# Kernel optimization log

Hardware: AMD Instinct MI355X
Metric: run time of the kernel (lower is better)

The kernel has to match this reference:

```python
import jax, jax.numpy as jnp
import numpy as np

B, S, D, H = 4, 2048, 768, 12
HD = D // H  # head_dim = 64


def setup_inputs() -> dict:
    key = jax.random.key(0)
    k1, k2, k3, k4, k5 = jax.random.split(key, 5)
    scale = 0.02
    return {
        "x": jax.random.normal(k1, (B, S, D), dtype=jnp.float32),
        "w_qkv": jax.random.normal(k2, (D, 3 * D), dtype=jnp.float32) * scale,
        "b_qkv": jax.random.normal(k3, (3 * D,), dtype=jnp.float32) * scale,
        "w_proj": jax.random.normal(k4, (D, D), dtype=jnp.float32) * scale,
        "b_proj": jax.random.normal(k5, (D,), dtype=jnp.float32) * scale,
    }


def reference(x, w_qkv, b_qkv, w_proj, b_proj):
    b, s, d = x.shape
    # fused qkv projection: (b, s, 3d) -> (3, b, h, s, hd)
    qkv = x @ w_qkv + b_qkv
    qkv = qkv.reshape(b, s, 3, H, HD).transpose(2, 0, 3, 1, 4)
    q, k, v = qkv[0], qkv[1], qkv[2]
    # scaled dot-product attention with explicit (b, h, s, s) scores
    scores = jnp.einsum("bhqd,bhkd->bhqk", q, k) / jnp.sqrt(jnp.float32(HD))
    attn = jax.nn.softmax(scores, axis=-1)
    out = jnp.einsum("bhqk,bhkd->bhqd", attn, v)
    out = out.transpose(0, 2, 1, 3).reshape(b, s, d)  # concat heads
    return out @ w_proj + b_proj
```

## Files before the change

### kernel.cpp

```cpp
#include <hip/hip_runtime.h>
#include <hip/hip_bf16.h>
#include <stdint.h>


typedef __attribute__((ext_vector_type(8))) short bf16x8;
typedef __attribute__((ext_vector_type(4))) float f32x4;
typedef __attribute__((ext_vector_type(4))) unsigned short u16x4;

__device__ __forceinline__ unsigned short f2bf(float x) {
  union { float f; uint32_t u; } v; v.f = x;
  uint32_t r = v.u + 0x7FFF + ((v.u >> 16) & 1);
  return (unsigned short)(r >> 16);
}

__device__ __forceinline__ uint32_t cvtpk_bf16(float lo, float hi) {
  uint32_t r;
  asm("v_cvt_pk_bf16_f32 %0, %1, %2" : "=v"(r) : "v"(lo), "v"(hi));
  return r;
}

__device__ __forceinline__ void gload_lds16(const void* g, void* l) {
  __builtin_amdgcn_global_load_lds(
      (const __attribute__((address_space(1))) void*)g,
      (__attribute__((address_space(3))) void*)l, 16, 0, 0);
}

__global__ void cast_x_kernel(const float* __restrict__ x,
                              unsigned short* __restrict__ xb, int n) {
  int idx = (blockIdx.x * blockDim.x + threadIdx.x) * 4;
  if (idx < n) {
    f32x4 v = *(const f32x4*)(x + idx);
    u16x4 o;
    o[0] = f2bf(v[0]); o[1] = f2bf(v[1]); o[2] = f2bf(v[2]); o[3] = f2bf(v[3]);
    *(u16x4*)(xb + idx) = o;
  }
}

__global__ void transpose_cast_kernel(const float* __restrict__ W,
                                      unsigned short* __restrict__ Wt,
                                      int K, int N) {
  __shared__ float tile[64][65];
  int k0 = blockIdx.y * 64, n0 = blockIdx.x * 64;
  int t = threadIdx.x;
#pragma unroll
  for (int i = 0; i < 16; i++) {
    int idx = i * 256 + t; int r = idx >> 6, c = idx & 63;
    tile[r][c] = W[(size_t)(k0 + r) * N + n0 + c];
  }
  __syncthreads();
#pragma unroll
  for (int i = 0; i < 16; i++) {
    int idx = i * 256 + t; int r = idx >> 6, c = idx & 63;
    Wt[(size_t)(n0 + r) * K + k0 + c] = f2bf(tile[c][r]);
  }
}

template <int EPI>
__global__ __launch_bounds__(256, 2) void gemm_kernel(
    const unsigned short* __restrict__ A,
    const unsigned short* __restrict__ Bt,
    const float* __restrict__ bias,
    void* __restrict__ out0,
    unsigned short* __restrict__ Kb,
    unsigned short* __restrict__ Vt,
    int M, int N, int K) {
  __shared__ unsigned short As[128 * 64];
  __shared__ unsigned short Bs[128 * 64];
  const int tid = threadIdx.x;
  const int wave = tid >> 6, lane = tid & 63;
  const int wm = wave >> 1, wn = wave & 1;
  const int m0 = blockIdx.y * 128, n0 = blockIdx.x * 128;
  const int g = lane >> 4, c16 = lane & 15;
  f32x4 acc[4][4] = {};

  for (int k0 = 0; k0 < K; k0 += 64) {
    int rb = wave * 32;
#pragma unroll
    for (int j = 0; j < 4; j++) {
      int r = rb + j * 8 + (lane >> 3);
      int ca = (lane & 7) ^ (r & 7);
      gload_lds16(A + (size_t)(m0 + r) * K + k0 + ca * 8, As + (rb + j * 8) * 64);
      gload_lds16(Bt + (size_t)(n0 + r) * K + k0 + ca * 8, Bs + (rb + j * 8) * 64);
    }
    __syncthreads();
#pragma unroll
    for (int ks = 0; ks < 2; ks++) {
      bf16x8 af[4], bfr[4];
#pragma unroll
      for (int mi = 0; mi < 4; mi++) {
        int row = wm * 64 + mi * 16 + c16;
        int ch = (ks * 4 + g) ^ (row & 7);
        af[mi] = *(const bf16x8*)(As + row * 64 + ch * 8);
      }
#pragma unroll
      for (int nj = 0; nj < 4; nj++) {
        int row = wn * 64 + nj * 16 + c16;
        int ch = (ks * 4 + g) ^ (row & 7);
        bfr[nj] = *(const bf16x8*)(Bs + row * 64 + ch * 8);
      }
#pragma unroll
      for (int mi = 0; mi < 4; mi++)
#pragma unroll
        for (int nj = 0; nj < 4; nj++)
          acc[mi][nj] = __builtin_amdgcn_mfma_f32_16x16x32_bf16(
              af[mi], bfr[nj], acc[mi][nj], 0, 0, 0);
    }
    __syncthreads();
  }

  if (EPI == 0) {
    const float QSC = 0.125f * 1.44269504088896f;
    unsigned short* Qb = (unsigned short*)out0;
#pragma unroll
    for (int nj = 0; nj < 4; nj++) {
      int n = n0 + wn * 64 + nj * 16 + c16;
      int t = n / 768, rr = n % 768;
      int h = rr >> 6, d = rr & 63;
      float bv = bias[n];
#pragma unroll
      for (int mi = 0; mi < 4; mi++) {
        int mrow = m0 + wm * 64 + mi * 16 + g * 4;
        int b = mrow >> 11, s = mrow & 2047;
        if (t == 0) {
          size_t base = ((size_t)(b * 12 + h) * 2048 + s) * 64 + d;
#pragma unroll
          for (int rg = 0; rg < 4; rg++)
            Qb[base + (size_t)rg * 64] = f2bf((acc[mi][nj][rg] + bv) * QSC);
        } else if (t == 1) {
          size_t base = ((size_t)(b * 12 + h) * 2048 + s) * 64 + d;
#pragma unroll
          for (int rg = 0; rg < 4; rg++)
            Kb[base + (size_t)rg * 64] = f2bf(acc[mi][nj][rg] + bv);
        } else {
          u16x4 p;
          p[0] = f2bf(acc[mi][nj][0] + bv);
          p[1] = f2bf(acc[mi][nj][1] + bv);
          p[2] = f2bf(acc[mi][nj][2] + bv);
          p[3] = f2bf(acc[mi][nj][3] + bv);
          *(u16x4*)(Vt + ((size_t)(b * 12 + h) * 64 + d) * 2048 + s) = p;
        }
      }
    }
  } else {
    float* outp = (float*)out0;
#pragma unroll
    for (int nj = 0; nj < 4; nj++) {
      int n = n0 + wn * 64 + nj * 16 + c16;
      float bv = bias[n];
#pragma unroll
      for (int mi = 0; mi < 4; mi++) {
        int mrow = m0 + wm * 64 + mi * 16 + g * 4;
#pragma unroll
        for (int rg = 0; rg < 4; rg++)
          outp[(size_t)(mrow + rg) * N + n] = acc[mi][nj][rg] + bv;
      }
    }
  }
}

__global__ __launch_bounds__(256, 4) void attn_kernel(
    const unsigned short* __restrict__ Qb,
    const unsigned short* __restrict__ Kb,
    const unsigned short* __restrict__ Vt,
    unsigned short* __restrict__ Ao) {
  __shared__ unsigned short Ks[64 * 64];
  __shared__ unsigned short Vs[64 * 64];
  __shared__ unsigned short Ps[4][2][16 * 72];
  const int bh = blockIdx.y;
  const int q0 = blockIdx.x * 128;
  const int tid = threadIdx.x;
  const int wave = tid >> 6, lane = tid & 63;
  const int g = lane >> 4, c16 = lane & 15;

  bf16x8 qf[2][2];
  {
    const unsigned short* qp =
        Qb + ((size_t)bh * 2048 + q0 + wave * 32 + c16) * 64;
#pragma unroll
    for (int qa = 0; qa < 2; qa++) {
      qf[qa][0] = *(const bf16x8*)(qp + qa * 1024 + g * 8);
      qf[qa][1] = *(const bf16x8*)(qp + qa * 1024 + 32 + g * 8);
    }
  }
  f32x4 acc_o[2][4] = {};
  float l_run[2] = {0.f, 0.f};
  const int alane = (lane & 48) + g * 4;
  const int rb = wave * 16;

  for (int kt = 0; kt < 32; kt++) {
#pragma unroll
    for (int j = 0; j < 2; j++) {
      int r = rb + j * 8 + (lane >> 3);
      int ca = (lane & 7) ^ (r & 7);
      gload_lds16(Kb + ((size_t)bh * 2048 + kt * 64 + r) * 64 + ca * 8,
                  Ks + (rb + j * 8) * 64);
      gload_lds16(Vt + ((size_t)bh * 64 + r) * 2048 + kt * 64 + ca * 8,
                  Vs + (rb + j * 8) * 64);
    }
    __syncthreads();

    f32x4 sacc[2][4] = {};
#pragma unroll
    for (int ks = 0; ks < 2; ks++) {
#pragma unroll
      for (int nf = 0; nf < 4; nf++) {
        int row = nf * 16 + c16;
        int ch = (ks * 4 + g) ^ (row & 7);
        bf16x8 kf = *(const bf16x8*)(Ks + row * 64 + ch * 8);
        sacc[0][nf] =
            __builtin_amdgcn_mfma_f32_16x16x32_bf16(kf, qf[0][ks], sacc[0][nf], 0, 0, 0);
        sacc[1][nf] =
            __builtin_amdgcn_mfma_f32_16x16x32_bf16(kf, qf[1][ks], sacc[1][nf], 0, 0, 0);
      }
    }

#pragma unroll
    for (int qa = 0; qa < 2; qa++) {
      float rs = 0.f;
#pragma unroll
      for (int nf = 0; nf < 4; nf++) {
        float e0 = __builtin_amdgcn_exp2f(sacc[qa][nf][0]);
        float e1 = __builtin_amdgcn_exp2f(sacc[qa][nf][1]);
        float e2 = __builtin_amdgcn_exp2f(sacc[qa][nf][2]);
        float e3 = __builtin_amdgcn_exp2f(sacc[qa][nf][3]);
        rs += (e0 + e1) + (e2 + e3);
        uint32_t w0 = cvtpk_bf16(e0, e1);
        uint32_t w1 = cvtpk_bf16(e2, e3);
        *(uint64_t*)(&Ps[wave][qa][c16 * 72 + nf * 16 + g * 4]) =
            (uint64_t)w0 | ((uint64_t)w1 << 32);
      }
      rs += __shfl_xor(rs, 16);
      rs += __shfl_xor(rs, 32);
      l_run[qa] += rs;
    }

#pragma unroll
    for (int ks = 0; ks < 2; ks++) {
      bf16x8 paf0 = *(const bf16x8*)(&Ps[wave][0][c16 * 72 + ks * 32 + g * 8]);
      bf16x8 paf1 = *(const bf16x8*)(&Ps[wave][1][c16 * 72 + ks * 32 + g * 8]);
#pragma unroll
      for (int nf = 0; nf < 4; nf++) {
        int row = nf * 16 + c16;
        int ch = (ks * 4 + g) ^ (row & 7);
        bf16x8 vf = *(const bf16x8*)(Vs + row * 64 + ch * 8);
        acc_o[0][nf] =
            __builtin_amdgcn_mfma_f32_16x16x32_bf16(paf0, vf, acc_o[0][nf], 0, 0, 0);
        acc_o[1][nf] =
            __builtin_amdgcn_mfma_f32_16x16x32_bf16(paf1, vf, acc_o[1][nf], 0, 0, 0);
      }
    }
    __syncthreads();
  }

  const int b = bh / 12, h = bh % 12;
#pragma unroll
  for (int qa = 0; qa < 2; qa++) {
    float l_q[4];
#pragma unroll
    for (int rg = 0; rg < 4; rg++)
      l_q[rg] = __shfl(l_run[qa], alane + rg);
#pragma unroll
    for (int nf = 0; nf < 4; nf++) {
#pragma unroll
      for (int rg = 0; rg < 4; rg++) {
        float v = acc_o[qa][nf][rg] / l_q[rg];
        int srow = q0 + wave * 32 + qa * 16 + g * 4 + rg;
        Ao[((size_t)(b * 2048 + srow)) * 768 + h * 64 + nf * 16 + c16] = f2bf(v);
      }
    }
  }
}

extern "C" void kernel_launch(void* const* d_in, const int* in_sizes, int n_in,
                              void* d_out, int out_size, void* d_ws, size_t ws_size,
                              hipStream_t stream) {
  const float* x      = (const float*)d_in[0];
  const float* w_qkv  = (const float*)d_in[1];
  const float* b_qkv  = (const float*)d_in[2];
  const float* w_proj = (const float*)d_in[3];
  const float* b_proj = (const float*)d_in[4];

  unsigned short* xb  = (unsigned short*)d_ws;
  unsigned short* wqt = xb + 6291456;
  unsigned short* wpt = wqt + 1769472;
  unsigned short* Qb  = wpt + 589824;
  unsigned short* Kb  = Qb + 6291456;
  unsigned short* Vt  = Kb + 6291456;
  unsigned short* Ao  = Vt + 6291456;

  cast_x_kernel<<<6144, 256, 0, stream>>>(x, xb, 6291456);
  transpose_cast_kernel<<<dim3(36, 12), 256, 0, stream>>>(w_qkv, wqt, 768, 2304);
  transpose_cast_kernel<<<dim3(12, 12), 256, 0, stream>>>(w_proj, wpt, 768, 768);

  gemm_kernel<0><<<dim3(18, 64), 256, 0, stream>>>(
      xb, wqt, b_qkv, (void*)Qb, Kb, Vt, 8192, 2304, 768);

  attn_kernel<<<dim3(16, 48), 256, 0, stream>>>(Qb, Kb, Vt, Ao);

  gemm_kernel<1><<<dim3(6, 64), 256, 0, stream>>>(
      Ao, wpt, b_proj, d_out, nullptr, nullptr, 8192, 768, 768);
}
```

Baseline: 154.0 us.

## Double-buffer K/V tiles in attention kernel to overlap loads with compute

```diff
diff --git a/kernel.cpp b/kernel.cpp
--- a/kernel.cpp
+++ b/kernel.cpp
@@ -163,14 +163,19 @@
     const unsigned short* __restrict__ Kb,
     const unsigned short* __restrict__ Vt,
     unsigned short* __restrict__ Ao) {
-  __shared__ unsigned short Ks[64 * 64];
-  __shared__ unsigned short Vs[64 * 64];
+  __shared__ unsigned short Ks[2][64 * 64];
+  __shared__ unsigned short Vs[2][64 * 64];
   __shared__ unsigned short Ps[4][2][16 * 72];
   const int bh = blockIdx.y;
   const int q0 = blockIdx.x * 128;
   const int tid = threadIdx.x;
   const int wave = tid >> 6, lane = tid & 63;
   const int g = lane >> 4, c16 = lane & 15;
+  const int rb = wave * 16;
+
+  const int sr = rb + (lane >> 3);
+  const int sca = (lane & 7) ^ (sr & 7);
+  const int sca1 = (lane & 7) ^ ((sr + 8) & 7);
 
   bf16x8 qf[2][2];
   {
@@ -185,19 +190,29 @@
   f32x4 acc_o[2][4] = {};
   float l_run[2] = {0.f, 0.f};
   const int alane = (lane & 48) + g * 4;
-  const int rb = wave * 16;
+
+  {
+    const unsigned short* kp = Kb + ((size_t)bh * 2048 + sr) * 64;
+    const unsigned short* vp = Vt + ((size_t)bh * 64 + sr) * 2048;
+    gload_lds16(kp + sca * 8, &Ks[0][(rb)*64]);
+    gload_lds16(kp + 8 * 64 + sca1 * 8, &Ks[0][(rb + 8) * 64]);
+    gload_lds16(vp + sca * 8, &Vs[0][(rb)*64]);
+    gload_lds16(vp + 8 * 2048 + sca1 * 8, &Vs[0][(rb + 8) * 64]);
+  }
+  __syncthreads();
 
   for (int kt = 0; kt < 32; kt++) {
-#pragma unroll
-    for (int j = 0; j < 2; j++) {
-      int r = rb + j * 8 + (lane >> 3);
-      int ca = (lane & 7) ^ (r & 7);
-      gload_lds16(Kb + ((size_t)bh * 2048 + kt * 64 + r) * 64 + ca * 8,
-                  Ks + (rb + j * 8) * 64);
-      gload_lds16(Vt + ((size_t)bh * 64 + r) * 2048 + kt * 64 + ca * 8,
-                  Vs + (rb + j * 8) * 64);
-    }
-    __syncthreads();
+    const int cur = kt & 1;
+    if (kt < 31) {
+      const unsigned short* kp =
+          Kb + ((size_t)bh * 2048 + (kt + 1) * 64 + sr) * 64;
+      const unsigned short* vp =
+          Vt + ((size_t)bh * 64 + sr) * 2048 + (kt + 1) * 64;
+      gload_lds16(kp + sca * 8, &Ks[cur ^ 1][(rb)*64]);
+      gload_lds16(kp + 8 * 64 + sca1 * 8, &Ks[cur ^ 1][(rb + 8) * 64]);
+      gload_lds16(vp + sca * 8, &Vs[cur ^ 1][(rb)*64]);
+      gload_lds16(vp + 8 * 2048 + sca1 * 8, &Vs[cur ^ 1][(rb + 8) * 64]);
+    }
 
     f32x4 sacc[2][4] = {};
 #pragma unroll
@@ -206,7 +221,7 @@
       for (int nf = 0; nf < 4; nf++) {
         int row = nf * 16 + c16;
         int ch = (ks * 4 + g) ^ (row & 7);
-        bf16x8 kf = *(const bf16x8*)(Ks + row * 64 + ch * 8);
+        bf16x8 kf = *(const bf16x8*)(&Ks[cur][row * 64 + ch * 8]);
         sacc[0][nf] =
             __builtin_amdgcn_mfma_f32_16x16x32_bf16(kf, qf[0][ks], sacc[0][nf], 0, 0, 0);
         sacc[1][nf] =
@@ -242,7 +257,7 @@
       for (int nf = 0; nf < 4; nf++) {
         int row = nf * 16 + c16;
         int ch = (ks * 4 + g) ^ (row & 7);
-        bf16x8 vf = *(const bf16x8*)(Vs + row * 64 + ch * 8);
+        bf16x8 vf = *(const bf16x8*)(&Vs[cur][row * 64 + ch * 8]);
         acc_o[0][nf] =
             __builtin_amdgcn_mfma_f32_16x16x32_bf16(paf0, vf, acc_o[0][nf], 0, 0, 0);
         acc_o[1][nf] =
```

Result: slower. 165.7 us (+7.6%).

## Double-buffer K/V tiles in attention kernel to overlap loads with compute

Applied to the files above, without the earlier changes.

```diff
diff --git a/kernel.cpp b/kernel.cpp
--- a/kernel.cpp
+++ b/kernel.cpp
@@ -158,19 +158,31 @@
   }
 }
 
-__global__ __launch_bounds__(256, 4) void attn_kernel(
+struct AttnState {
+  f32x4 acc_o[2][4];
+  float l_run[2];
+};
+
+__global__ __launch_bounds__(256, 3) void attn_kernel(
     const unsigned short* __restrict__ Qb,
     const unsigned short* __restrict__ Kb,
     const unsigned short* __restrict__ Vt,
     unsigned short* __restrict__ Ao) {
-  __shared__ unsigned short Ks[64 * 64];
-  __shared__ unsigned short Vs[64 * 64];
+  __shared__ unsigned short Ks0[64 * 64];
+  __shared__ unsigned short Ks1[64 * 64];
+  __shared__ unsigned short Vs0[64 * 64];
+  __shared__ unsigned short Vs1[64 * 64];
   __shared__ unsigned short Ps[4][2][16 * 72];
   const int bh = blockIdx.y;
   const int q0 = blockIdx.x * 128;
   const int tid = threadIdx.x;
   const int wave = tid >> 6, lane = tid & 63;
   const int g = lane >> 4, c16 = lane & 15;
+  const int rb = wave * 16;
+
+  const int sr = rb + (lane >> 3);
+  const int sca = (lane & 7) ^ (sr & 7);
+  const int sca1 = (lane & 7) ^ ((sr + 8) & 7);
 
   bf16x8 qf[2][2];
   {
@@ -185,72 +197,80 @@
   f32x4 acc_o[2][4] = {};
   float l_run[2] = {0.f, 0.f};
   const int alane = (lane & 48) + g * 4;
-  const int rb = wave * 16;
-
-  for (int kt = 0; kt < 32; kt++) {
-#pragma unroll
-    for (int j = 0; j < 2; j++) {
-      int r = rb + j * 8 + (lane >> 3);
-      int ca = (lane & 7) ^ (r & 7);
-      gload_lds16(Kb + ((size_t)bh * 2048 + kt * 64 + r) * 64 + ca * 8,
-                  Ks + (rb + j * 8) * 64);
-      gload_lds16(Vt + ((size_t)bh * 64 + r) * 2048 + kt * 64 + ca * 8,
-                  Vs + (rb + j * 8) * 64);
-    }
+
+  const unsigned short* kp = Kb + ((size_t)bh * 2048 + sr) * 64;
+  const unsigned short* vp = Vt + ((size_t)bh * 64 + sr) * 2048;
+
+#define STAGE_KV(KS, VS)                                   \
+  do {                                                     \
+    gload_lds16(kp + sca * 8, &KS[rb * 64]);               \
+    gload_lds16(kp + 8 * 64 + sca1 * 8, &KS[(rb + 8) * 64]); \
+    gload_lds16(vp + sca * 8, &VS[rb * 64]);               \
+    gload_lds16(vp + 8 * 2048 + sca1 * 8, &VS[(rb + 8) * 64]); \
+    kp += 64 * 64;                                         \
+    vp += 64;                                              \
+  } while (0)
+
+#define ATTN_TILE(KS, VS)                                                     \
+  do {                                                                        \
+    f32x4 sacc[2][4] = {};                                                    \
+    _Pragma("unroll") for (int ks = 0; ks < 2; ks++) {                        \
+      _Pragma("unroll") for (int nf = 0; nf < 4; nf++) {                      \
+        int row = nf * 16 + c16;                                              \
+        int ch = (ks * 4 + g) ^ (row & 7);                                    \
+        bf16x8 kf = *(const bf16x8*)(&KS[row * 64 + ch * 8]);                 \
+        sacc[0][nf] = __builtin_amdgcn_mfma_f32_16x16x32_bf16(                \
+            kf, qf[0][ks], sacc[0][nf], 0, 0, 0);                             \
+        sacc[1][nf] = __builtin_amdgcn_mfma_f32_16x16x32_bf16(                \
+            kf, qf[1][ks], sacc[1][nf], 0, 0, 0);                             \
+      }                                                                       \
+    }                                                                         \
+    _Pragma("unroll") for (int qa = 0; qa < 2; qa++) {                        \
+      float rs = 0.f;                                                         \
+      _Pragma("unroll") for (int nf = 0; nf < 4; nf++) {                      \
+        float e0 = __builtin_amdgcn_exp2f(sacc[qa][nf][0]);                   \
+        float e1 = __builtin_amdgcn_exp2f(sacc[qa][nf][1]);                   \
+        float e2 = __builtin_amdgcn_exp2f(sacc[qa][nf][2]);                   \
+        float e3 = __builtin_amdgcn_exp2f(sacc[qa][nf][3]);                   \
+        rs += (e0 + e1) + (e2 + e3);                                          \
+        uint32_t w0 = cvtpk_bf16(e0, e1);                                     \
+        uint32_t w1 = cvtpk_bf16(e2, e3);                                     \
+        *(uint64_t*)(&Ps[wave][qa][c16 * 72 + nf * 16 + g * 4]) =             \
+            (uint64_t)w0 | ((uint64_t)w1 << 32);                              \
+      }                                                                       \
+      rs += __shfl_xor(rs, 16);                                               \
+      rs += __shfl_xor(rs, 32);                                               \
+      l_run[qa] += rs;                                                        \
+    }                                                                         \
+    _Pragma("unroll") for (int ks = 0; ks < 2; ks++) {                        \
+      bf16x8 paf0 = *(const bf16x8*)(&Ps[wave][0][c16 * 72 + ks * 32 + g * 8]); \
+      bf16x8 paf1 = *(const bf16x8*)(&Ps[wave][1][c16 * 72 + ks * 32 + g * 8]); \
+      _Pragma("unroll") for (int nf = 0; nf < 4; nf++) {                      \
+        int row = nf * 16 + c16;                                              \
+        int ch = (ks * 4 + g) ^ (row & 7);                                    \
+        bf16x8 vf = *(const bf16x8*)(&VS[row * 64 + ch * 8]);                 \
+        acc_o[0][nf] = __builtin_amdgcn_mfma_f32_16x16x32_bf16(               \
+            paf0, vf, acc_o[0][nf], 0, 0, 0);                                 \
+        acc_o[1][nf] = __builtin_amdgcn_mfma_f32_16x16x32_bf16(               \
+            paf1, vf, acc_o[1][nf], 0, 0, 0);                                 \
+      }                                                                       \
+    }                                                                         \
+  } while (0)
+
+  STAGE_KV(Ks0, Vs0);
+  __syncthreads();
+
+  for (int kt2 = 0; kt2 < 16; kt2++) {
+    STAGE_KV(Ks1, Vs1);
+    ATTN_TILE(Ks0, Vs0);
     __syncthreads();
 
-    f32x4 sacc[2][4] = {};
-#pragma unroll
-    for (int ks = 0; ks < 2; ks++) {
-#pragma unroll
-      for (int nf = 0; nf < 4; nf++) {
-        int row = nf * 16 + c16;
-        int ch = (ks * 4 + g) ^ (row & 7);
-        bf16x8 kf = *(const bf16x8*)(Ks + row * 64 + ch * 8);
-        sacc[0][nf] =
-            __builtin_amdgcn_mfma_f32_16x16x32_bf16(kf, qf[0][ks], sacc[0][nf], 0, 0, 0);
-        sacc[1][nf] =
-            __builtin_amdgcn_mfma_f32_16x16x32_bf16(kf, qf[1][ks], sacc[1][nf], 0, 0, 0);
-      }
-    }
-
-#pragma unroll
-    for (int qa = 0; qa < 2; qa++) {
-      float rs = 0.f;
-#pragma unroll
-      for (int nf = 0; nf < 4; nf++) {
-        float e0 = __builtin_amdgcn_exp2f(sacc[qa][nf][0]);
-        float e1 = __builtin_amdgcn_exp2f(sacc[qa][nf][1]);
-        float e2 = __builtin_amdgcn_exp2f(sacc[qa][nf][2]);
-        float e3 = __builtin_amdgcn_exp2f(sacc[qa][nf][3]);
-        rs += (e0 + e1) + (e2 + e3);
-        uint32_t w0 = cvtpk_bf16(e0, e1);
-        uint32_t w1 = cvtpk_bf16(e2, e3);
-        *(uint64_t*)(&Ps[wave][qa][c16 * 72 + nf * 16 + g * 4]) =
-            (uint64_t)w0 | ((uint64_t)w1 << 32);
-      }
-      rs += __shfl_xor(rs, 16);
-      rs += __shfl_xor(rs, 32);
-      l_run[qa] += rs;
-    }
-
-#pragma unroll
-    for (int ks = 0; ks < 2; ks++) {
-      bf16x8 paf0 = *(const bf16x8*)(&Ps[wave][0][c16 * 72 + ks * 32 + g * 8]);
-      bf16x8 paf1 = *(const bf16x8*)(&Ps[wave][1][c16 * 72 + ks * 32 + g * 8]);
-#pragma unroll
-      for (int nf = 0; nf < 4; nf++) {
-        int row = nf * 16 + c16;
-        int ch = (ks * 4 + g) ^ (row & 7);
-        bf16x8 vf = *(const bf16x8*)(Vs + row * 64 + ch * 8);
-        acc_o[0][nf] =
-            __builtin_amdgcn_mfma_f32_16x16x32_bf16(paf0, vf, acc_o[0][nf], 0, 0, 0);
-        acc_o[1][nf] =
-            __builtin_amdgcn_mfma_f32_16x16x32_bf16(paf1, vf, acc_o[1][nf], 0, 0, 0);
-      }
-    }
+    if (kt2 < 15) STAGE_KV(Ks0, Vs0);
+    ATTN_TILE(Ks1, Vs1);
     __syncthreads();
   }
+#undef STAGE_KV
+#undef ATTN_TILE
 
   const int b = bh / 12, h = bh % 12;
 #pragma unroll
```

New measurement: 168.4 us. 9.3% more time.

## Keep softmax probabilities in registers, permuting V reads to match MFMA layout

Applied to the files above, without the earlier changes.

```diff
diff --git a/kernel.cpp b/kernel.cpp
--- a/kernel.cpp
+++ b/kernel.cpp
@@ -4,6 +4,7 @@
 
 
 typedef __attribute__((ext_vector_type(8))) short bf16x8;
+typedef __attribute__((ext_vector_type(4))) short bf16x4;
 typedef __attribute__((ext_vector_type(4))) float f32x4;
 typedef __attribute__((ext_vector_type(4))) unsigned short u16x4;
 
@@ -165,12 +166,13 @@
     unsigned short* __restrict__ Ao) {
   __shared__ unsigned short Ks[64 * 64];
   __shared__ unsigned short Vs[64 * 64];
-  __shared__ unsigned short Ps[4][2][16 * 72];
   const int bh = blockIdx.y;
   const int q0 = blockIdx.x * 128;
   const int tid = threadIdx.x;
   const int wave = tid >> 6, lane = tid & 63;
   const int g = lane >> 4, c16 = lane & 15;
+  const int rw = c16 & 7;
+  const int rb = wave * 16;
 
   bf16x8 qf[2][2];
   {
@@ -185,7 +187,6 @@
   f32x4 acc_o[2][4] = {};
   float l_run[2] = {0.f, 0.f};
   const int alane = (lane & 48) + g * 4;
-  const int rb = wave * 16;
 
   for (int kt = 0; kt < 32; kt++) {
 #pragma unroll
@@ -219,15 +220,12 @@
       float rs = 0.f;
 #pragma unroll
       for (int nf = 0; nf < 4; nf++) {
-        float e0 = __builtin_amdgcn_exp2f(sacc[qa][nf][0]);
-        float e1 = __builtin_amdgcn_exp2f(sacc[qa][nf][1]);
-        float e2 = __builtin_amdgcn_exp2f(sacc[qa][nf][2]);
-        float e3 = __builtin_amdgcn_exp2f(sacc[qa][nf][3]);
-        rs += (e0 + e1) + (e2 + e3);
-        uint32_t w0 = cvtpk_bf16(e0, e1);
-        uint32_t w1 = cvtpk_bf16(e2, e3);
-        *(uint64_t*)(&Ps[wave][qa][c16 * 72 + nf * 16 + g * 4]) =
-            (uint64_t)w0 | ((uint64_t)w1 << 32);
+        sacc[qa][nf][0] = __builtin_amdgcn_exp2f(sacc[qa][nf][0]);
+        sacc[qa][nf][1] = __builtin_amdgcn_exp2f(sacc[qa][nf][1]);
+        sacc[qa][nf][2] = __builtin_amdgcn_exp2f(sacc[qa][nf][2]);
+        sacc[qa][nf][3] = __builtin_amdgcn_exp2f(sacc[qa][nf][3]);
+        rs += (sacc[qa][nf][0] + sacc[qa][nf][1]) +
+              (sacc[qa][nf][2] + sacc[qa][nf][3]);
       }
       rs += __shfl_xor(rs, 16);
       rs += __shfl_xor(rs, 32);
@@ -236,17 +234,27 @@
 
 #pragma unroll
     for (int ks = 0; ks < 2; ks++) {
-      bf16x8 paf0 = *(const bf16x8*)(&Ps[wave][0][c16 * 72 + ks * 32 + g * 8]);
-      bf16x8 paf1 = *(const bf16x8*)(&Ps[wave][1][c16 * 72 + ks * 32 + g * 8]);
+      union { uint32_t w[4]; bf16x8 v8; } pa0, pa1;
+      pa0.w[0] = cvtpk_bf16(sacc[0][2 * ks][0], sacc[0][2 * ks][1]);
+      pa0.w[1] = cvtpk_bf16(sacc[0][2 * ks][2], sacc[0][2 * ks][3]);
+      pa0.w[2] = cvtpk_bf16(sacc[0][2 * ks + 1][0], sacc[0][2 * ks + 1][1]);
+      pa0.w[3] = cvtpk_bf16(sacc[0][2 * ks + 1][2], sacc[0][2 * ks + 1][3]);
+      pa1.w[0] = cvtpk_bf16(sacc[1][2 * ks][0], sacc[1][2 * ks][1]);
+      pa1.w[1] = cvtpk_bf16(sacc[1][2 * ks][2], sacc[1][2 * ks][3]);
+      pa1.w[2] = cvtpk_bf16(sacc[1][2 * ks + 1][0], sacc[1][2 * ks + 1][1]);
+      pa1.w[3] = cvtpk_bf16(sacc[1][2 * ks + 1][2], sacc[1][2 * ks + 1][3]);
+      const int c_lo = ks * 4 + (g >> 1);
+      const int hwo = (g & 1) * 4;
 #pragma unroll
       for (int nf = 0; nf < 4; nf++) {
         int row = nf * 16 + c16;
-        int ch = (ks * 4 + g) ^ (row & 7);
-        bf16x8 vf = *(const bf16x8*)(Vs + row * 64 + ch * 8);
+        union { struct { bf16x4 lo, hi; } h; bf16x8 v8; } vf;
+        vf.h.lo = *(const bf16x4*)(&Vs[row * 64 + (c_lo ^ rw) * 8 + hwo]);
+        vf.h.hi = *(const bf16x4*)(&Vs[row * 64 + ((c_lo + 2) ^ rw) * 8 + hwo]);
         acc_o[0][nf] =
-            __builtin_amdgcn_mfma_f32_16x16x32_bf16(paf0, vf, acc_o[0][nf], 0, 0, 0);
+            __builtin_amdgcn_mfma_f32_16x16x32_bf16(pa0.v8, vf.v8, acc_o[0][nf], 0, 0, 0);
         acc_o[1][nf] =
-            __builtin_amdgcn_mfma_f32_16x16x32_bf16(paf1, vf, acc_o[1][nf], 0, 0, 0);
+            __builtin_amdgcn_mfma_f32_16x16x32_bf16(pa1.v8, vf.v8, acc_o[1][nf], 0, 0, 0);
       }
     }
     __syncthreads();
```

After: 153.9 us. Within noise of the previous version (-0.1%).
